# Optimization experiments

Measured on AMD Instinct MI355X. Metric: run time of the kernel, lower is better.

The kernel has to match this reference:

```python
import jax, jax.numpy as jnp
import numpy as np

B, T, NF, D = 32, 128, 20, 512
S = 5            # num_sample
L = 96           # seq_len per utterance (static)
EPS = 1e-8


def _cosine(a, b):
    # torch.F.cosine_similarity: dot / max(|a|*|b|, eps)
    num = jnp.sum(a * b, axis=-1)
    den = jnp.maximum(
        jnp.sqrt(jnp.sum(a * a, axis=-1)) * jnp.sqrt(jnp.sum(b * b, axis=-1)), EPS
    )
    return num / den


def setup_inputs() -> dict:
    key = jax.random.key(0)
    output = jax.random.normal(key, (B, T, NF, D), dtype=jnp.float32)

    # static segment gather indices: seq_len = L for every utterance
    batch_idx = jnp.asarray(np.repeat(np.arange(B), L), dtype=jnp.int32)
    time_idx = jnp.asarray(np.tile(np.arange(L), B), dtype=jnp.int32)

    # negative frame indices: for anchor frame i, sample S frames from
    # {0..NF-1} \ {i-1, i, i+1} (matches masked randperm sampling)
    rng = np.random.default_rng(0)
    neg = np.empty((NF - 1, S), dtype=np.int32)
    all_f = np.arange(NF)
    for i in range(NF - 1):
        allowed = all_f[(all_f != i - 1) & (all_f != i) & (all_f != i + 1)]
        neg[i] = rng.permutation(allowed)[:S]
    neg_idx = jnp.asarray(neg.reshape(-1), dtype=jnp.int32)  # [(NF-1)*S]

    return {"output": output, "batch_idx": batch_idx, "time_idx": time_idx,
            "neg_idx": neg_idx}


def reference(output, batch_idx, time_idx, neg_idx):
    # gather valid segments: [num_seg, NF, D]
    seg = output[batch_idx, time_idx]

    anchors = seg[:, :-1, :]                      # [num_seg, NF-1, D]
    sim_pos = _cosine(anchors, seg[:, 1:, :])     # [num_seg, NF-1]

    # negatives[seg, i, s] = seg[seg, neg_idx[i*S+s]]
    negs = seg[:, neg_idx, :].reshape(seg.shape[0], NF - 1, S, D)
    sim_neg = _cosine(anchors[:, :, None, :], negs)          # [num_seg, NF-1, S]

    sim_all = jnp.concatenate([sim_pos[..., None], sim_neg], axis=-1)
    loss = jnp.mean(-jax.nn.log_softmax(sim_all, axis=-1)[..., 0])
    return loss
```

## Files before the change

### kernel.cpp

```cpp
#include <hip/hip_runtime.h>
#include <hip/hip_bf16.h>
#include <math.h>

#define B_  32
#define T_  128
#define NF_ 20
#define D_  512
#define S_  5
#define L_  96
#define EPS_ 1e-8f
#define NSEG (B_ * L_)
#define NPOS (NF_ - 1)
#define NELEM (NF_ * D_)
#define RPAD (D_ + 8)
#define GLD 33

typedef short short8 __attribute__((ext_vector_type(8)));
typedef float f32x4  __attribute__((ext_vector_type(4)));

__device__ __forceinline__ unsigned f2bf2(float lo, float hi) {
  unsigned ulo = __float_as_uint(lo);
  ulo += 0x7fffu + ((ulo >> 16) & 1u);
  unsigned uhi = __float_as_uint(hi);
  uhi += 0x7fffu + ((uhi >> 16) & 1u);
  return (uhi & 0xffff0000u) | (ulo >> 16);
}

__global__ __launch_bounds__(256) void phoneme_ssl_seg_kernel(
    const float* __restrict__ out,
    const int* __restrict__ batch_idx,
    const int* __restrict__ time_idx,
    const int* __restrict__ neg_idx,
    float* __restrict__ partials) {

  __shared__ __align__(16) unsigned short V[NF_ * RPAD];
  __shared__ float G[32 * GLD];

  const int n = blockIdx.x;
  const int b = batch_idx[n];
  const int t = time_idx[n];
  const float* __restrict__ src = out + (size_t)(b * T_ + t) * NELEM;

  const float4* __restrict__ src4 = (const float4*)src;
#pragma unroll
  for (int it = 0; it < 5; ++it) {
    const int c = threadIdx.x + 256 * it;
    const float4 x = src4[2 * c];
    const float4 y = src4[2 * c + 1];
    uint4 w;
    w.x = f2bf2(x.x, x.y);
    w.y = f2bf2(x.z, x.w);
    w.z = f2bf2(y.x, y.y);
    w.w = f2bf2(y.z, y.w);
    const int row = c >> 6;
    const int col = (c & 63) * 8;
    *(uint4*)&V[row * RPAD + col] = w;
  }
  __syncthreads();

  {
    const int wave = threadIdx.x >> 6;
    const int lane = threadIdx.x & 63;
    const int r = lane & 15;
    const int q = lane >> 4;
    const int rowA = (wave >= 2) ? ((16 + r > 19) ? 19 : 16 + r) : r;
    const int rowB = (wave & 1)  ? ((16 + r > 19) ? 19 : 16 + r) : r;
    const unsigned short* pA = &V[rowA * RPAD + q * 8];
    const unsigned short* pB = &V[rowB * RPAD + q * 8];
    f32x4 acc = {0.f, 0.f, 0.f, 0.f};
#pragma unroll
    for (int ks = 0; ks < D_ / 32; ++ks) {
      const short8 a = *(const short8*)(pA + 32 * ks);
      const short8 bb = (wave == 0 || wave == 3)
                          ? a
                          : *(const short8*)(pB + 32 * ks);
      acc = __builtin_amdgcn_mfma_f32_16x16x32_bf16(a, bb, acc, 0, 0, 0);
    }
    const int rbase = (wave >= 2) ? 16 : 0;
    const int cbase = (wave & 1) ? 16 : 0;
#pragma unroll
    for (int reg = 0; reg < 4; ++reg)
      G[(rbase + q * 4 + reg) * GLD + cbase + r] = acc[reg];
  }
  __syncthreads();
  if (threadIdx.x >= 64) return;

  float local = 0.f;
  if (threadIdx.x < NPOS) {
    const int i = threadIdx.x;
    const float na = sqrtf(G[i * GLD + i]);
    float sims[1 + S_];
    {
      const float nb = sqrtf(G[(i + 1) * GLD + (i + 1)]);
      sims[0] = G[i * GLD + (i + 1)] / fmaxf(na * nb, EPS_);
    }
#pragma unroll
    for (int j = 0; j < S_; ++j) {
      const int f = neg_idx[i * S_ + j];
      const float nb = sqrtf(G[f * GLD + f]);
      sims[1 + j] = G[i * GLD + f] / fmaxf(na * nb, EPS_);
    }
    float m = sims[0];
#pragma unroll
    for (int j = 1; j < 1 + S_; ++j) m = fmaxf(m, sims[j]);
    float se = 0.f;
#pragma unroll
    for (int j = 0; j < 1 + S_; ++j) se += __expf(sims[j] - m);
    const float lse = m + __logf(se);
    local = -(sims[0] - lse);
  }

#pragma unroll
  for (int off = 32; off >= 1; off >>= 1)
    local += __shfl_xor(local, off, 64);
  if (threadIdx.x == 0)
    partials[n] = local;
}

__global__ __launch_bounds__(256) void phoneme_ssl_reduce_kernel(
    const float* __restrict__ partials, float* __restrict__ loss_out) {
  float acc = 0.f;
  for (int i = threadIdx.x; i < NSEG; i += 256) acc += partials[i];
#pragma unroll
  for (int off = 32; off >= 1; off >>= 1)
    acc += __shfl_xor(acc, off, 64);
  __shared__ float ws[4];
  if ((threadIdx.x & 63) == 0) ws[threadIdx.x >> 6] = acc;
  __syncthreads();
  if (threadIdx.x == 0)
    loss_out[0] = (ws[0] + ws[1] + ws[2] + ws[3]) * (1.0f / (float)(NSEG * NPOS));
}

extern "C" void kernel_launch(void* const* d_in, const int* in_sizes, int n_in,
                              void* d_out, int out_size, void* d_ws, size_t ws_size,
                              hipStream_t stream) {
  const float* out_t    = (const float*)d_in[0];
  const int* batch_idx  = (const int*)d_in[1];
  const int* time_idx   = (const int*)d_in[2];
  const int* neg_idx    = (const int*)d_in[3];
  float* loss_out       = (float*)d_out;
  float* partials       = (float*)d_ws;

  phoneme_ssl_seg_kernel<<<NSEG, 256, 0, stream>>>(
      out_t, batch_idx, time_idx, neg_idx, partials);
  phoneme_ssl_reduce_kernel<<<1, 256, 0, stream>>>(partials, loss_out);
}
```

Measured before the change: 228.2 us.

## Process four segments per block with double-buffered register prefetch

Each block now handles four segments instead of one. While the MFMA Gram matrix of the current segment is computed, the next segment's fp32 data is loaded into registers, then converted to bf16 into a second LDS buffer. The Gram matrix buffer is also double-buffered, and the negative indices are loaded once per block. The aim is to hide global-load latency and amortize per-block setup, at the cost of four times fewer blocks and double the LDS per block, which lowers occupancy and the number of loads in flight.

```diff
diff --git a/kernel.cpp b/kernel.cpp
--- a/kernel.cpp
+++ b/kernel.cpp
@@ -14,6 +14,8 @@
 #define NELEM (NF_ * D_)
 #define RPAD (D_ + 8)
 #define GLD 33
+#define SPB 4
+#define NBLK (NSEG / SPB)
 
 typedef short short8 __attribute__((ext_vector_type(8)));
 typedef float f32x4  __attribute__((ext_vector_type(4)));
@@ -33,94 +35,128 @@
     const int* __restrict__ neg_idx,
     float* __restrict__ partials) {
 
-  __shared__ __align__(16) unsigned short V[NF_ * RPAD];
-  __shared__ float G[32 * GLD];
+  __shared__ __align__(16) unsigned short V[2][NF_ * RPAD];
+  __shared__ float G[2][32 * GLD];
 
-  const int n = blockIdx.x;
-  const int b = batch_idx[n];
-  const int t = time_idx[n];
-  const float* __restrict__ src = out + (size_t)(b * T_ + t) * NELEM;
+  const int wave = threadIdx.x >> 6;
+  const int lane = threadIdx.x & 63;
+  const int r = lane & 15;
+  const int q = lane >> 4;
+  const int rowA = (wave >= 2) ? ((16 + r > 19) ? 19 : 16 + r) : r;
+  const int rowB = (wave & 1)  ? ((16 + r > 19) ? 19 : 16 + r) : r;
+  const int rbase = (wave >= 2) ? 16 : 0;
+  const int cbase = (wave & 1) ? 16 : 0;
 
-  const float4* __restrict__ src4 = (const float4*)src;
+  int nidx[S_];
+  if (threadIdx.x < NPOS) {
 #pragma unroll
-  for (int it = 0; it < 5; ++it) {
-    const int c = threadIdx.x + 256 * it;
-    const float4 x = src4[2 * c];
-    const float4 y = src4[2 * c + 1];
-    uint4 w;
-    w.x = f2bf2(x.x, x.y);
-    w.y = f2bf2(x.z, x.w);
-    w.z = f2bf2(y.x, y.y);
-    w.w = f2bf2(y.z, y.w);
-    const int row = c >> 6;
-    const int col = (c & 63) * 8;
-    *(uint4*)&V[row * RPAD + col] = w;
+    for (int j = 0; j < S_; ++j) nidx[j] = neg_idx[threadIdx.x * S_ + j];
+  }
+
+  {
+    const int n0 = blockIdx.x * SPB;
+    const float4* __restrict__ src4 =
+        (const float4*)(out + (size_t)(batch_idx[n0] * T_ + time_idx[n0]) * NELEM);
+#pragma unroll
+    for (int it = 0; it < 5; ++it) {
+      const int c = threadIdx.x + 256 * it;
+      const float4 x = src4[2 * c];
+      const float4 y = src4[2 * c + 1];
+      uint4 w;
+      w.x = f2bf2(x.x, x.y); w.y = f2bf2(x.z, x.w);
+      w.z = f2bf2(y.x, y.y); w.w = f2bf2(y.z, y.w);
+      *(uint4*)&V[0][(c >> 6) * RPAD + (c & 63) * 8] = w;
+    }
   }
   __syncthreads();
 
-  {
-    const int wave = threadIdx.x >> 6;
-    const int lane = threadIdx.x & 63;
-    const int r = lane & 15;
-    const int q = lane >> 4;
-    const int rowA = (wave >= 2) ? ((16 + r > 19) ? 19 : 16 + r) : r;
-    const int rowB = (wave & 1)  ? ((16 + r > 19) ? 19 : 16 + r) : r;
-    const unsigned short* pA = &V[rowA * RPAD + q * 8];
-    const unsigned short* pB = &V[rowB * RPAD + q * 8];
-    f32x4 acc = {0.f, 0.f, 0.f, 0.f};
+  float local = 0.f;
 #pragma unroll
-    for (int ks = 0; ks < D_ / 32; ++ks) {
-      const short8 a = *(const short8*)(pA + 32 * ks);
-      const short8 bb = (wave == 0 || wave == 3)
-                          ? a
-                          : *(const short8*)(pB + 32 * ks);
-      acc = __builtin_amdgcn_mfma_f32_16x16x32_bf16(a, bb, acc, 0, 0, 0);
+  for (int s = 0; s < SPB; ++s) {
+    const int cur = s & 1, nxt = cur ^ 1;
+
+    float4 pf[10];
+    if (s + 1 < SPB) {
+      const int n1 = blockIdx.x * SPB + s + 1;
+      const float4* __restrict__ src4 =
+          (const float4*)(out + (size_t)(batch_idx[n1] * T_ + time_idx[n1]) * NELEM);
+#pragma unroll
+      for (int it = 0; it < 5; ++it) {
+        const int c = threadIdx.x + 256 * it;
+        pf[2 * it]     = src4[2 * c];
+        pf[2 * it + 1] = src4[2 * c + 1];
+      }
     }
-    const int rbase = (wave >= 2) ? 16 : 0;
-    const int cbase = (wave & 1) ? 16 : 0;
+
+    {
+      const unsigned short* pA = &V[cur][rowA * RPAD + q * 8];
+      const unsigned short* pB = &V[cur][rowB * RPAD + q * 8];
+      f32x4 acc = {0.f, 0.f, 0.f, 0.f};
 #pragma unroll
-    for (int reg = 0; reg < 4; ++reg)
-      G[(rbase + q * 4 + reg) * GLD + cbase + r] = acc[reg];
-  }
-  __syncthreads();
-  if (threadIdx.x >= 64) return;
+      for (int ks = 0; ks < D_ / 32; ++ks) {
+        const short8 a = *(const short8*)(pA + 32 * ks);
+        const short8 bb = (wave == 0 || wave == 3)
+                            ? a : *(const short8*)(pB + 32 * ks);
+        acc = __builtin_amdgcn_mfma_f32_16x16x32_bf16(a, bb, acc, 0, 0, 0);
+      }
+#pragma unroll
+      for (int reg = 0; reg < 4; ++reg)
+        G[cur][(rbase + q * 4 + reg) * GLD + cbase + r] = acc[reg];
+    }
 
-  float local = 0.f;
-  if (threadIdx.x < NPOS) {
-    const int i = threadIdx.x;
-    const float na = sqrtf(G[i * GLD + i]);
-    float sims[1 + S_];
-    {
-      const float nb = sqrtf(G[(i + 1) * GLD + (i + 1)]);
-      sims[0] = G[i * GLD + (i + 1)] / fmaxf(na * nb, EPS_);
+    if (s + 1 < SPB) {
+#pragma unroll
+      for (int it = 0; it < 5; ++it) {
+        const int c = threadIdx.x + 256 * it;
+        uint4 w;
+        w.x = f2bf2(pf[2 * it].x,     pf[2 * it].y);
+        w.y = f2bf2(pf[2 * it].z,     pf[2 * it].w);
+        w.z = f2bf2(pf[2 * it + 1].x, pf[2 * it + 1].y);
+        w.w = f2bf2(pf[2 * it + 1].z, pf[2 * it + 1].w);
+        *(uint4*)&V[nxt][(c >> 6) * RPAD + (c & 63) * 8] = w;
+      }
     }
+
+    __syncthreads();
+
+    if (threadIdx.x < NPOS) {
+      const int i = threadIdx.x;
+      const float* __restrict__ Gc = G[cur];
+      const float na = sqrtf(Gc[i * GLD + i]);
+      float sims[1 + S_];
+      {
+        const float nb = sqrtf(Gc[(i + 1) * GLD + (i + 1)]);
+        sims[0] = Gc[i * GLD + (i + 1)] / fmaxf(na * nb, EPS_);
+      }
 #pragma unroll
-    for (int j = 0; j < S_; ++j) {
-      const int f = neg_idx[i * S_ + j];
-      const float nb = sqrtf(G[f * GLD + f]);
-      sims[1 + j] = G[i * GLD + f] / fmaxf(na * nb, EPS_);
+      for (int j = 0; j < S_; ++j) {
+        const int f = nidx[j];
+        const float nb = sqrtf(Gc[f * GLD + f]);
+        sims[1 + j] = Gc[i * GLD + f] / fmaxf(na * nb, EPS_);
+      }
+      float m = sims[0];
+#pragma unroll
+      for (int j = 1; j < 1 + S_; ++j) m = fmaxf(m, sims[j]);
+      float se = 0.f;
+#pragma unroll
+      for (int j = 0; j < 1 + S_; ++j) se += __expf(sims[j] - m);
+      local += -(sims[0] - (m + __logf(se)));
     }
-    float m = sims[0];
-#pragma unroll
-    for (int j = 1; j < 1 + S_; ++j) m = fmaxf(m, sims[j]);
-    float se = 0.f;
-#pragma unroll
-    for (int j = 0; j < 1 + S_; ++j) se += __expf(sims[j] - m);
-    const float lse = m + __logf(se);
-    local = -(sims[0] - lse);
   }
 
+  if (threadIdx.x < 64) {
 #pragma unroll
-  for (int off = 32; off >= 1; off >>= 1)
-    local += __shfl_xor(local, off, 64);
-  if (threadIdx.x == 0)
-    partials[n] = local;
+    for (int off = 32; off >= 1; off >>= 1)
+      local += __shfl_xor(local, off, 64);
+    if (threadIdx.x == 0)
+      partials[blockIdx.x] = local;
+  }
 }
 
 __global__ __launch_bounds__(256) void phoneme_ssl_reduce_kernel(
     const float* __restrict__ partials, float* __restrict__ loss_out) {
   float acc = 0.f;
-  for (int i = threadIdx.x; i < NSEG; i += 256) acc += partials[i];
+  for (int i = threadIdx.x; i < NBLK; i += 256) acc += partials[i];
 #pragma unroll
   for (int off = 32; off >= 1; off >>= 1)
     acc += __shfl_xor(acc, off, 64);
@@ -141,7 +177,7 @@
   float* loss_out       = (float*)d_out;
   float* partials       = (float*)d_ws;
 
-  phoneme_ssl_seg_kernel<<<NSEG, 256, 0, stream>>>(
+  phoneme_ssl_seg_kernel<<<NBLK, 256, 0, stream>>>(
       out_t, batch_idx, time_idx, neg_idx, partials);
   phoneme_ssl_reduce_kernel<<<1, 256, 0, stream>>>(partials, loss_out);
 }
```

After: 228.3 us. Within noise of the previous version (+0.0%).

## Assign one wave per segment and feed MFMA directly from global loads

Applied to the files above, without the earlier changes.

Each wave now handles one segment, so a block covers four segments. Each wave loads its 20 rows straight from global memory into registers, converts them to bf16 and runs three MFMA tiles (00, 01, 11) to build the Gram matrix. This drops the LDS staging buffer and one block-wide barrier. The next k-slice is software-prefetched while the current one computes. In exchange, rows 16-19 are loaded redundantly by duplicate lanes and register pressure per wave goes up.

```diff
diff --git a/kernel.cpp b/kernel.cpp
--- a/kernel.cpp
+++ b/kernel.cpp
@@ -12,8 +12,9 @@
 #define NSEG (B_ * L_)
 #define NPOS (NF_ - 1)
 #define NELEM (NF_ * D_)
-#define RPAD (D_ + 8)
-#define GLD 33
+#define SPB 4
+#define NBLK (NSEG / SPB)
+#define GLD 21
 
 typedef short short8 __attribute__((ext_vector_type(8)));
 typedef float f32x4  __attribute__((ext_vector_type(4)));
@@ -26,6 +27,13 @@
   return (uhi & 0xffff0000u) | (ulo >> 16);
 }
 
+__device__ __forceinline__ short8 pack8(float4 x, float4 y) {
+  uint4 u;
+  u.x = f2bf2(x.x, x.y); u.y = f2bf2(x.z, x.w);
+  u.z = f2bf2(y.x, y.y); u.w = f2bf2(y.z, y.w);
+  return __builtin_bit_cast(short8, u);
+}
+
 __global__ __launch_bounds__(256) void phoneme_ssl_seg_kernel(
     const float* __restrict__ out,
     const int* __restrict__ batch_idx,
@@ -33,72 +41,73 @@
     const int* __restrict__ neg_idx,
     float* __restrict__ partials) {
 
-  __shared__ __align__(16) unsigned short V[NF_ * RPAD];
-  __shared__ float G[32 * GLD];
+  __shared__ float G[SPB][NF_ * GLD];
+  __shared__ float ws[SPB];
 
-  const int n = blockIdx.x;
-  const int b = batch_idx[n];
-  const int t = time_idx[n];
-  const float* __restrict__ src = out + (size_t)(b * T_ + t) * NELEM;
+  const int wave = threadIdx.x >> 6;
+  const int lane = threadIdx.x & 63;
+  const int r = lane & 15;
+  const int q = lane >> 4;
 
-  const float4* __restrict__ src4 = (const float4*)src;
+  const int n = blockIdx.x * SPB + wave;
+  const float4* __restrict__ src4 =
+      (const float4*)(out + (size_t)(batch_idx[n] * T_ + time_idx[n]) * NELEM);
+
+  const int r1 = (16 + r > 19) ? 19 : 16 + r;
+  const int o0 = r  * 128 + q * 2;
+  const int o1 = r1 * 128 + q * 2;
+
+  f32x4 c00 = {0.f, 0.f, 0.f, 0.f}, c01 = c00, c11 = c00;
+
+  float4 A0a = src4[o0], A0b = src4[o0 + 1];
+  float4 A1a = src4[o1], A1b = src4[o1 + 1];
 #pragma unroll
-  for (int it = 0; it < 5; ++it) {
-    const int c = threadIdx.x + 256 * it;
-    const float4 x = src4[2 * c];
-    const float4 y = src4[2 * c + 1];
-    uint4 w;
-    w.x = f2bf2(x.x, x.y);
-    w.y = f2bf2(x.z, x.w);
-    w.z = f2bf2(y.x, y.y);
-    w.w = f2bf2(y.z, y.w);
-    const int row = c >> 6;
-    const int col = (c & 63) * 8;
-    *(uint4*)&V[row * RPAD + col] = w;
+  for (int ks = 0; ks < D_ / 32; ++ks) {
+    float4 N0a, N0b, N1a, N1b;
+    if (ks < 15) {
+      const int oo = (ks + 1) * 8;
+      N0a = src4[o0 + oo]; N0b = src4[o0 + oo + 1];
+      N1a = src4[o1 + oo]; N1b = src4[o1 + oo + 1];
+    }
+    const short8 a0 = pack8(A0a, A0b);
+    const short8 a1 = pack8(A1a, A1b);
+    c00 = __builtin_amdgcn_mfma_f32_16x16x32_bf16(a0, a0, c00, 0, 0, 0);
+    c01 = __builtin_amdgcn_mfma_f32_16x16x32_bf16(a0, a1, c01, 0, 0, 0);
+    c11 = __builtin_amdgcn_mfma_f32_16x16x32_bf16(a1, a1, c11, 0, 0, 0);
+    if (ks < 15) { A0a = N0a; A0b = N0b; A1a = N1a; A1b = N1b; }
+  }
+
+  {
+    float* __restrict__ Gw = G[wave];
+#pragma unroll
+    for (int reg = 0; reg < 4; ++reg) {
+      const int m = q * 4 + reg;
+      Gw[m * GLD + r] = c00[reg];
+      if (r < 4) {
+        Gw[m * GLD + 16 + r]   = c01[reg];
+        Gw[(16 + r) * GLD + m] = c01[reg];
+        if (q == 0)
+          Gw[(16 + reg) * GLD + 16 + r] = c11[reg];
+      }
+    }
   }
   __syncthreads();
 
-  {
-    const int wave = threadIdx.x >> 6;
-    const int lane = threadIdx.x & 63;
-    const int r = lane & 15;
-    const int q = lane >> 4;
-    const int rowA = (wave >= 2) ? ((16 + r > 19) ? 19 : 16 + r) : r;
-    const int rowB = (wave & 1)  ? ((16 + r > 19) ? 19 : 16 + r) : r;
-    const unsigned short* pA = &V[rowA * RPAD + q * 8];
-    const unsigned short* pB = &V[rowB * RPAD + q * 8];
-    f32x4 acc = {0.f, 0.f, 0.f, 0.f};
-#pragma unroll
-    for (int ks = 0; ks < D_ / 32; ++ks) {
-      const short8 a = *(const short8*)(pA + 32 * ks);
-      const short8 bb = (wave == 0 || wave == 3)
-                          ? a
-                          : *(const short8*)(pB + 32 * ks);
-      acc = __builtin_amdgcn_mfma_f32_16x16x32_bf16(a, bb, acc, 0, 0, 0);
-    }
-    const int rbase = (wave >= 2) ? 16 : 0;
-    const int cbase = (wave & 1) ? 16 : 0;
-#pragma unroll
-    for (int reg = 0; reg < 4; ++reg)
-      G[(rbase + q * 4 + reg) * GLD + cbase + r] = acc[reg];
-  }
-  __syncthreads();
-  if (threadIdx.x >= 64) return;
-
   float local = 0.f;
-  if (threadIdx.x < NPOS) {
-    const int i = threadIdx.x;
-    const float na = sqrtf(G[i * GLD + i]);
+  if (lane < NPOS) {
+    const int i = lane;
+    const float* __restrict__ Gc = G[wave];
+    const float na = sqrtf(Gc[i * GLD + i]);
     float sims[1 + S_];
     {
-      const float nb = sqrtf(G[(i + 1) * GLD + (i + 1)]);
-      sims[0] = G[i * GLD + (i + 1)] / fmaxf(na * nb, EPS_);
+      const float nb = sqrtf(Gc[(i + 1) * GLD + (i + 1)]);
+      sims[0] = Gc[i * GLD + (i + 1)] / fmaxf(na * nb, EPS_);
     }
 #pragma unroll
     for (int j = 0; j < S_; ++j) {
       const int f = neg_idx[i * S_ + j];
-      const float nb = sqrtf(G[f * GLD + f]);
-      sims[1 + j] = G[i * GLD + f] / fmaxf(na * nb, EPS_);
+      const float nb = sqrtf(Gc[f * GLD + f]);
+      sims[1 + j] = Gc[i * GLD + f] / fmaxf(na * nb, EPS_);
     }
     float m = sims[0];
 #pragma unroll
@@ -106,21 +115,22 @@
     float se = 0.f;
 #pragma unroll
     for (int j = 0; j < 1 + S_; ++j) se += __expf(sims[j] - m);
-    const float lse = m + __logf(se);
-    local = -(sims[0] - lse);
+    local = -(sims[0] - (m + __logf(se)));
   }
 
 #pragma unroll
   for (int off = 32; off >= 1; off >>= 1)
     local += __shfl_xor(local, off, 64);
+  if (lane == 0) ws[wave] = local;
+  __syncthreads();
   if (threadIdx.x == 0)
-    partials[n] = local;
+    partials[blockIdx.x] = ws[0] + ws[1] + ws[2] + ws[3];
 }
 
 __global__ __launch_bounds__(256) void phoneme_ssl_reduce_kernel(
     const float* __restrict__ partials, float* __restrict__ loss_out) {
   float acc = 0.f;
-  for (int i = threadIdx.x; i < NSEG; i += 256) acc += partials[i];
+  for (int i = threadIdx.x; i < NBLK; i += 256) acc += partials[i];
 #pragma unroll
   for (int off = 32; off >= 1; off >>= 1)
     acc += __shfl_xor(acc, off, 64);
@@ -141,7 +151,7 @@
   float* loss_out       = (float*)d_out;
   float* partials       = (float*)d_ws;
 
-  phoneme_ssl_seg_kernel<<<NSEG, 256, 0, stream>>>(
+  phoneme_ssl_seg_kernel<<<NBLK, 256, 0, stream>>>(
       out_t, batch_idx, time_idx, neg_idx, partials);
   phoneme_ssl_reduce_kernel<<<1, 256, 0, stream>>>(partials, loss_out);
 }
```

New measurement: 229.4 us. About the same (+0.5%).
